# Performance work log

Measured on AMD Instinct MI355X. Metric: run time of the kernel, lower is better.

The kernel has to match this reference:

```python
import jax, jax.numpy as jnp
import numpy as np

N_EMBD = 2048
HIDDEN = 2 * N_EMBD        # 4096
ADAPT = HIDDEN // 16       # 256
B, S = 4, 2048


def _layernorm(x, g, b, eps=1e-5):
    mu = jnp.mean(x, axis=-1, keepdims=True)
    var = jnp.var(x, axis=-1, keepdims=True)
    return (x - mu) * jax.lax.rsqrt(var + eps) * g + b


def setup_inputs() -> dict:
    key = jax.random.key(0)
    ks = jax.random.split(key, 7)
    scale = 1.0 / np.sqrt(N_EMBD)
    adapt_scale = scale * 0.01
    return {
        "x": jax.random.normal(ks[0], (B, S, N_EMBD), dtype=jnp.float32),
        "W_up": jax.random.normal(ks[1], (HIDDEN, N_EMBD), dtype=jnp.float32) * scale,
        "W_gate": jax.random.normal(ks[2], (HIDDEN, N_EMBD), dtype=jnp.float32) * scale,
        "W_down": jax.random.normal(ks[3], (N_EMBD, HIDDEN), dtype=jnp.float32) * scale,
        "W_pre": jax.random.normal(ks[4], (ADAPT, N_EMBD), dtype=jnp.float32) * adapt_scale,
        "W_post": jax.random.normal(ks[5], (ADAPT, HIDDEN), dtype=jnp.float32) * adapt_scale,
        "W_proj": jax.random.normal(ks[6], (HIDDEN, ADAPT), dtype=jnp.float32) * adapt_scale,
        "ln_g": jnp.ones((ADAPT,), dtype=jnp.float32),
        "ln_b": jnp.zeros((ADAPT,), dtype=jnp.float32),
    }


def reference(x, W_up, W_gate, W_down, W_pre, W_post, W_proj, ln_g, ln_b):
    # SwiGLU trunk
    up = jnp.einsum('bsd,hd->bsh', x, W_up)
    gate = jnp.einsum('bsd,hd->bsh', x, W_gate)
    hidden = jax.nn.silu(gate) * up                      # [B,S,H]
    # Low-rank quadratic adapter
    adapt_in = _layernorm(jnp.einsum('bsd,ad->bsa', x, W_pre), ln_g, ln_b)       # [B,S,A]
    adapt_out = _layernorm(jnp.einsum('bsh,ah->bsa', hidden, W_post), ln_g, ln_b)  # [B,S,A]
    aw = jnp.einsum('bsa,bta->bst', adapt_in, adapt_out)  # [B,S,S]
    aw = jax.nn.silu(jnp.clip(aw, -5.0, 5.0))
    adapt = jnp.einsum('bst,bta->bsa', aw, adapt_in)      # [B,S,A]
    adapt = 0.1 * jnp.einsum('bsa,ha->bsh', adapt, W_proj)
    hidden = hidden + adapt
    out = jnp.einsum('bsh,dh->bsd', hidden, W_down)       # dropout p=0 -> identity
    return out
```

## Files before the change

kernel.cpp:

```cpp
#include <hip/hip_runtime.h>
#include <cstdint>
#include <cstddef>

typedef unsigned short u16;
typedef short short8 __attribute__((ext_vector_type(8)));
typedef float f32x4 __attribute__((ext_vector_type(4)));

__device__ __forceinline__ u16 f2bf(float f) {
  union { float f; unsigned u; } x; x.f = f;
  unsigned r = x.u + 0x7FFFu + ((x.u >> 16) & 1u);
  return (u16)(r >> 16);
}
__device__ __forceinline__ float b2f(u16 h) {
  union { unsigned u; float f; } x; x.u = ((unsigned)h) << 16;
  return x.f;
}
__device__ __forceinline__ float silu_f(float v) {
  return v / (1.f + __expf(-v));
}
__device__ __forceinline__ void gll(const u16* g, u16* l) {
  __builtin_amdgcn_global_load_lds((const __attribute__((address_space(1))) unsigned*)g,
                                   (__attribute__((address_space(3))) unsigned*)l, 16, 0, 0);
}
__device__ __forceinline__ short8 ld8(const u16* p) { return *(const short8*)p; }

__global__ __launch_bounds__(256) void cvt7_k(const float4* __restrict__ s0,
                                              const float4* __restrict__ s1,
                                              const float4* __restrict__ s2,
                                              const float4* __restrict__ s3,
                                              const float4* __restrict__ s4,
                                              const float4* __restrict__ s5,
                                              ushort4* __restrict__ dst) {
  const int i = blockIdx.x * 256 + threadIdx.x;
  const int o1 = 4194304, o2 = 6291456, o3 = 8388608, o4 = 10485760,
            o5 = 10616832, o6 = 10878976;
  if (i >= o6) return;
  const float4* src;
  int base;
  if      (i < o1) { src = s0; base = 0;  }
  else if (i < o2) { src = s1; base = o1; }
  else if (i < o3) { src = s2; base = o2; }
  else if (i < o4) { src = s3; base = o3; }
  else if (i < o5) { src = s4; base = o4; }
  else             { src = s5; base = o5; }
  float4 v = src[i - base];
  ushort4 o;
  o.x = f2bf(v.x); o.y = f2bf(v.y); o.z = f2bf(v.z); o.w = f2bf(v.w);
  dst[i] = o;
}

__global__ __launch_bounds__(256) void tcvt_k(const float* __restrict__ in,
                                              u16* __restrict__ out) {
  const int h = blockIdx.x, a = threadIdx.x;
  out[(size_t)a * 4096 + h] = f2bf(in[(size_t)h * 256 + a]);
}

__global__ __launch_bounds__(256) void red_ln_k(const float* __restrict__ part,
                                                const float* __restrict__ g,
                                                const float* __restrict__ b,
                                                u16* __restrict__ out,
                                                u16* __restrict__ outT, int Mtot) {
  const int row = blockIdx.x;
  const int a = threadIdx.x;
  const size_t stride = (size_t)Mtot * 256;
  const size_t base = (size_t)row * 256 + a;
  float v = part[base] + part[base + stride] + part[base + 2 * stride] + part[base + 3 * stride];
  float s = v, s2 = v * v;
#pragma unroll
  for (int o = 32; o; o >>= 1) { s += __shfl_down(s, o, 64); s2 += __shfl_down(s2, o, 64); }
  __shared__ float red[8];
  int l = a & 63, w = a >> 6;
  if (l == 0) { red[w] = s; red[4 + w] = s2; }
  __syncthreads();
  s  = red[0] + red[1] + red[2] + red[3];
  s2 = red[4] + red[5] + red[6] + red[7];
  float mu  = s * 0.00390625f;
  float var = s2 * 0.00390625f - mu * mu;
  float rs  = rsqrtf(var + 1e-5f);
  float o   = (v - mu) * rs * g[a] + b[a];
  u16 ob = f2bf(o);
  out[base] = ob;
  if (outT) {
    int bi = row >> 11, t = row & 2047;
    outT[((size_t)bi * 256 + a) * 2048 + t] = ob;
  }
}

__global__ __launch_bounds__(256) void red_k(const float* __restrict__ part,
                                             u16* __restrict__ out, int Mtot, float scale) {
  const int row = blockIdx.x;
  const int a = threadIdx.x;
  const size_t stride = (size_t)Mtot * 256;
  const size_t base = (size_t)row * 256 + a;
  float v = part[base] + part[base + stride] + part[base + 2 * stride] + part[base + 3 * stride];
  out[base] = f2bf(v * scale);
}

template <int EPI>
__global__ __launch_bounds__(256) void gemm_bt(const u16* __restrict__ A,
                                               const u16* __restrict__ B,
                                               void* __restrict__ Cv,
                                               int M, int N, int K,
                                               long bA, long bB, long bC) {
  __shared__ u16 Al[128 * 64];
  __shared__ u16 Bl[128 * 64];
  const int tid  = threadIdx.x;
  const int bz   = blockIdx.z;
  const int brow = blockIdx.y * 128;
  const int bcol = blockIdx.x * 128;
  A += (size_t)bz * bA;
  B += (size_t)bz * bB;
  const int lane = tid & 63;
  const int w = tid >> 6, wr = w >> 1, wc = w & 1;
  const int srow = tid >> 3;
  const int scol = (tid & 7) * 8;

  f32x4 acc[4][4] = {};

  for (int kt = 0; kt < K; kt += 64) {
#pragma unroll
    for (int i = 0; i < 4; ++i)
      gll(A + (size_t)(brow + i * 32 + srow) * K + kt + scol, &Al[(i * 256 + tid) * 8]);
#pragma unroll
    for (int i = 0; i < 4; ++i)
      gll(B + (size_t)(bcol + i * 32 + srow) * K + kt + scol, &Bl[(i * 256 + tid) * 8]);
    __syncthreads();
#pragma unroll
    for (int kk = 0; kk < 2; ++kk) {
      short8 af[4], bfr[4];
      const int ko = kk * 32 + (lane >> 4) * 8;
#pragma unroll
      for (int m = 0; m < 4; ++m)
        af[m] = *(const short8*)&Al[(wr * 64 + m * 16 + (lane & 15)) * 64 + ko];
#pragma unroll
      for (int n = 0; n < 4; ++n)
        bfr[n] = *(const short8*)&Bl[(wc * 64 + n * 16 + (lane & 15)) * 64 + ko];
#pragma unroll
      for (int m = 0; m < 4; ++m)
#pragma unroll
        for (int n = 0; n < 4; ++n)
          acc[m][n] = __builtin_amdgcn_mfma_f32_16x16x32_bf16(af[m], bfr[n], acc[m][n], 0, 0, 0);
    }
    __syncthreads();
  }

  const int col0 = bcol + wc * 64 + (lane & 15);
  const int row0 = brow + wr * 64 + ((lane >> 4) << 2);
  u16* Cb = (u16*)Cv + (size_t)bz * bC;
#pragma unroll
  for (int m = 0; m < 4; ++m)
#pragma unroll
    for (int j = 0; j < 4; ++j) {
      size_t roff = (size_t)(row0 + m * 16 + j) * N + col0;
#pragma unroll
      for (int n = 0; n < 4; ++n) {
        float v = acc[m][n][j];
        if (EPI == 2) {
          v = fminf(5.f, fmaxf(-5.f, v));
          v = silu_f(v);
        }
        Cb[roff + n * 16] = f2bf(v);
      }
    }
}

__global__ __launch_bounds__(256) void gemm_sk(const u16* __restrict__ A,
                                               const u16* __restrict__ B,
                                               float* __restrict__ part,
                                               int M, int N, int Kfull, int Kc,
                                               long bA, long bB, int Mtot) {
  const int z  = blockIdx.z;
  const int b  = z >> 2, sk = z & 3;
  const int brow = blockIdx.y * 128;
  const int bcol = blockIdx.x * 128;
  A += (size_t)b * bA + (size_t)sk * Kc;
  B += (size_t)b * bB + (size_t)sk * Kc;

  __shared__ u16 Al[128 * 64];
  __shared__ u16 Bl[128 * 64];
  const int tid  = threadIdx.x;
  const int lane = tid & 63;
  const int w = tid >> 6, wr = w >> 1, wc = w & 1;
  const int srow = tid >> 3;
  const int scol = (tid & 7) * 8;

  f32x4 acc[4][4] = {};

  for (int kt = 0; kt < Kc; kt += 64) {
#pragma unroll
    for (int i = 0; i < 4; ++i)
      gll(A + (size_t)(brow + i * 32 + srow) * Kfull + kt + scol, &Al[(i * 256 + tid) * 8]);
#pragma unroll
    for (int i = 0; i < 4; ++i)
      gll(B + (size_t)(bcol + i * 32 + srow) * Kfull + kt + scol, &Bl[(i * 256 + tid) * 8]);
    __syncthreads();
#pragma unroll
    for (int kk = 0; kk < 2; ++kk) {
      short8 af[4], bfr[4];
      const int ko = kk * 32 + (lane >> 4) * 8;
#pragma unroll
      for (int m = 0; m < 4; ++m)
        af[m] = *(const short8*)&Al[(wr * 64 + m * 16 + (lane & 15)) * 64 + ko];
#pragma unroll
      for (int n = 0; n < 4; ++n)
        bfr[n] = *(const short8*)&Bl[(wc * 64 + n * 16 + (lane & 15)) * 64 + ko];
#pragma unroll
      for (int m = 0; m < 4; ++m)
#pragma unroll
        for (int n = 0; n < 4; ++n)
          acc[m][n] = __builtin_amdgcn_mfma_f32_16x16x32_bf16(af[m], bfr[n], acc[m][n], 0, 0, 0);
    }
    __syncthreads();
  }

  const int col0 = bcol + wc * 64 + (lane & 15);
  const int row0 = brow + wr * 64 + ((lane >> 4) << 2);
  float* P = part + ((size_t)sk * Mtot + (size_t)b * M) * N;
#pragma unroll
  for (int m = 0; m < 4; ++m)
#pragma unroll
    for (int j = 0; j < 4; ++j) {
      size_t roff = (size_t)(row0 + m * 16 + j) * N + col0;
#pragma unroll
      for (int n = 0; n < 4; ++n) P[roff + n * 16] = acc[m][n][j];
    }
}

__device__ __forceinline__ void pipe256(const u16* Abase, const u16* Bbase, int K,
                                        u16* As, u16* Bs, int tid, int wm, int wn,
                                        int lane, f32x4 (*acc)[4]) {
  const int fr  = lane & 15;
  const int cs0 = ((((lane >> 4) << 4) ^ ((lane & 7) << 4)) >> 1);
  const int cs1 = cs0 ^ 32;
  const int NT = K >> 6;

  auto stage = [&](const u16* OPb, u16* L, int tt, int half) {
    const u16* s = OPb + (size_t)(half * 128) * K + (tt << 6);
    u16* d = &L[((tt & 1) * 2 + half) * 8192 + tid * 8];
    gll(s, d); gll(s + (size_t)64 * K, d + 4096);
  };

  stage(Abase, As, 0, 0); stage(Bbase, Bs, 0, 0);
  stage(Abase, As, 0, 1); stage(Bbase, Bs, 0, 1);
  if (NT > 1) {
    stage(Abase, As, 1, 0); stage(Bbase, Bs, 1, 0);
    stage(Abase, As, 1, 1); stage(Bbase, Bs, 1, 1);
    asm volatile("s_waitcnt vmcnt(8)" ::: "memory");
  } else {
    asm volatile("s_waitcnt vmcnt(0)" ::: "memory");
  }
  __builtin_amdgcn_s_barrier();

  const int aoff0 = (wm * 64 + fr) * 64;
  const int boff0 = (wn * 32 + fr) * 64;

  short8 aLo[8], aHi[8], bb[4];

  for (int t = 0; t < NT; ++t) {
    const u16* h0a = &As[(t & 1) * 16384];
    const u16* h0b = &Bs[(t & 1) * 16384];
    const u16* h1a = h0a + 8192;
    const u16* h1b = h0b + 8192;
    const bool pf = (t + 2 < NT);

#pragma unroll
    for (int m = 0; m < 4; ++m) {
      aLo[m * 2]     = ld8(h0a + aoff0 + m * 1024 + cs0);
      aLo[m * 2 + 1] = ld8(h0a + aoff0 + m * 1024 + cs1);
    }
#pragma unroll
    for (int n = 0; n < 2; ++n) {
      bb[n * 2]     = ld8(h0b + boff0 + n * 1024 + cs0);
      bb[n * 2 + 1] = ld8(h0b + boff0 + n * 1024 + cs1);
    }
    __builtin_amdgcn_s_barrier();
    asm volatile("s_waitcnt lgkmcnt(0)" ::: "memory");
    __builtin_amdgcn_s_setprio(1);
#pragma unroll
    for (int m = 0; m < 4; ++m)
#pragma unroll
      for (int n = 0; n < 2; ++n) {
        acc[m][n] = __builtin_amdgcn_mfma_f32_16x16x32_bf16(aLo[m*2],   bb[n*2],   acc[m][n], 0, 0, 0);
        acc[m][n] = __builtin_amdgcn_mfma_f32_16x16x32_bf16(aLo[m*2+1], bb[n*2+1], acc[m][n], 0, 0, 0);
      }
    __builtin_amdgcn_s_setprio(0);
    __builtin_amdgcn_s_barrier();

#pragma unroll
    for (int m = 0; m < 4; ++m) {
      aHi[m * 2]     = ld8(h1a + aoff0 + m * 1024 + cs0);
      aHi[m * 2 + 1] = ld8(h1a + aoff0 + m * 1024 + cs1);
    }
    if (pf) { stage(Abase, As, t + 2, 0); stage(Bbase, Bs, t + 2, 0); }
    __builtin_amdgcn_s_barrier();
    asm volatile("s_waitcnt lgkmcnt(0)" ::: "memory");
    __builtin_amdgcn_s_setprio(1);
#pragma unroll
    for (int m = 0; m < 4; ++m)
#pragma unroll
      for (int n = 0; n < 2; ++n) {
        acc[4+m][n] = __builtin_amdgcn_mfma_f32_16x16x32_bf16(aHi[m*2],   bb[n*2],   acc[4+m][n], 0, 0, 0);
        acc[4+m][n] = __builtin_amdgcn_mfma_f32_16x16x32_bf16(aHi[m*2+1], bb[n*2+1], acc[4+m][n], 0, 0, 0);
      }
    __builtin_amdgcn_s_setprio(0);
    __builtin_amdgcn_s_barrier();

#pragma unroll
    for (int n = 0; n < 2; ++n) {
      bb[n * 2]     = ld8(h1b + boff0 + n * 1024 + cs0);
      bb[n * 2 + 1] = ld8(h1b + boff0 + n * 1024 + cs1);
    }
    if (pf) stage(Abase, As, t + 2, 1);
    __builtin_amdgcn_s_barrier();
    asm volatile("s_waitcnt lgkmcnt(0)" ::: "memory");
    __builtin_amdgcn_s_setprio(1);
#pragma unroll
    for (int m = 0; m < 4; ++m)
#pragma unroll
      for (int n = 0; n < 2; ++n) {
        acc[m][2+n] = __builtin_amdgcn_mfma_f32_16x16x32_bf16(aLo[m*2],   bb[n*2],   acc[m][2+n], 0, 0, 0);
        acc[m][2+n] = __builtin_amdgcn_mfma_f32_16x16x32_bf16(aLo[m*2+1], bb[n*2+1], acc[m][2+n], 0, 0, 0);
      }
    __builtin_amdgcn_s_setprio(0);
    __builtin_amdgcn_s_barrier();

    if (pf) stage(Bbase, Bs, t + 2, 1);
    __builtin_amdgcn_s_barrier();
    asm volatile("s_waitcnt lgkmcnt(0)" ::: "memory");
    __builtin_amdgcn_s_setprio(1);
#pragma unroll
    for (int m = 0; m < 4; ++m)
#pragma unroll
      for (int n = 0; n < 2; ++n) {
        acc[4+m][2+n] = __builtin_amdgcn_mfma_f32_16x16x32_bf16(aHi[m*2],   bb[n*2],   acc[4+m][2+n], 0, 0, 0);
        acc[4+m][2+n] = __builtin_amdgcn_mfma_f32_16x16x32_bf16(aHi[m*2+1], bb[n*2+1], acc[4+m][2+n], 0, 0, 0);
      }
    __builtin_amdgcn_s_setprio(0);
    if (t + 2 < NT)      { asm volatile("s_waitcnt vmcnt(8)" ::: "memory"); }
    else if (t + 1 < NT) { asm volatile("s_waitcnt vmcnt(0)" ::: "memory"); }
    __builtin_amdgcn_s_barrier();
  }
}

template <int EPI>
__global__ __launch_bounds__(512, 2) void gemm256(const u16* __restrict__ A,
                                                  const u16* __restrict__ B,
                                                  void* __restrict__ Cv,
                                                  const u16* __restrict__ H,
                                                  int N, int K,
                                                  const u16* __restrict__ A2,
                                                  const u16* __restrict__ B2, int K2) {
  __shared__ __align__(16) u16 As[32768];
  __shared__ __align__(16) u16 Bs[32768];
  const int tid = threadIdx.x;

  const int gx = gridDim.x;
  const int nwg = gx * gridDim.y;
  int orig = blockIdx.y * gx + blockIdx.x;
  {
    int q = nwg >> 3, r = nwg & 7;
    int xcd = orig & 7, idx = orig >> 3;
    orig = (xcd < r) ? xcd * (q + 1) + idx : r * (q + 1) + (xcd - r) * q + idx;
  }
  const int brow = (orig / gx) * 256;
  const int bcol = (orig % gx) * 256;

  const int lane = tid & 63;
  const int wid  = tid >> 6;
  const int wm = wid >> 2, wn = wid & 3;
  const int srow = tid >> 3;
  const int scol = ((((tid & 7) << 4) ^ ((srow & 7) << 4)) >> 1);

  f32x4 acc[8][4] = {};

  pipe256(A + (size_t)(brow + srow) * K + scol,
          B + (size_t)(bcol + srow) * K + scol, K, As, Bs, tid, wm, wn, lane, acc);
  if (K2 > 0)
    pipe256(A2 + (size_t)(brow + srow) * K2 + scol,
            B2 + (size_t)(bcol + srow) * K2 + scol, K2, As, Bs, tid, wm, wn, lane, acc);

  const int fr = lane & 15;
#pragma unroll
  for (int m = 0; m < 8; ++m) {
    const int mrow = (m < 4) ? (wm * 64 + m * 16) : (128 + wm * 64 + (m - 4) * 16);
#pragma unroll
    for (int j = 0; j < 4; ++j) {
      const size_t roff = (size_t)(brow + mrow + ((lane >> 4) << 2) + j) * N + bcol + fr;
#pragma unroll
      for (int n = 0; n < 4; ++n) {
        const int ncol = (n < 2) ? (wn * 32 + n * 16) : (128 + wn * 32 + (n - 2) * 16);
        const size_t idx = roff + ncol;
        if (EPI == 0) {
          ((float*)Cv)[idx] = acc[m][n][j];
        } else if (EPI == 1) {
          ((u16*)Cv)[idx] = f2bf(acc[m][n][j]);
        } else {
          ((u16*)Cv)[idx] = f2bf(silu_f(acc[m][n][j]) * b2f(H[idx]));
        }
      }
    }
  }
}

extern "C" void kernel_launch(void* const* d_in, const int* in_sizes, int n_in,
                              void* d_out, int out_size, void* d_ws, size_t ws_size,
                              hipStream_t stream) {
  const float* x      = (const float*)d_in[0];
  const float* W_up   = (const float*)d_in[1];
  const float* W_gate = (const float*)d_in[2];
  const float* W_down = (const float*)d_in[3];
  const float* W_pre  = (const float*)d_in[4];
  const float* W_post = (const float*)d_in[5];
  const float* W_proj = (const float*)d_in[6];
  const float* ln_g   = (const float*)d_in[7];
  const float* ln_b   = (const float*)d_in[8];
  (void)in_sizes; (void)n_in; (void)out_size; (void)ws_size;

  const int D = 2048, Hh = 4096, A_ = 256, Bn = 4, S = 2048, M = 8192;

  char* p = (char*)d_ws;
  u16* xb      = (u16*)p; p += (size_t)M * D * 2;
  u16* Wup_b   = (u16*)p; p += (size_t)Hh * D * 2;
  u16* Wgate_b = (u16*)p; p += (size_t)Hh * D * 2;
  u16* Wdown_b = (u16*)p; p += (size_t)D * Hh * 2;
  u16* Wpre_b  = (u16*)p; p += (size_t)A_ * D * 2;
  u16* Wpost_b = (u16*)p; p += (size_t)A_ * Hh * 2;
  u16* WprojT  = (u16*)p; p += (size_t)Hh * A_ * 2;
  u16* hidden  = (u16*)p; p += (size_t)M * Hh * 2;
  u16* scratch = (u16*)p; p += (size_t)M * Hh * 2;
  char* q = (char*)scratch;
  u16*   aw        = (u16*)q; q += (size_t)Bn * S * S * 2;
  u16*   adapt_in  = (u16*)q; q += (size_t)M * A_ * 2;
  u16*   adapt_inT = (u16*)q; q += (size_t)M * A_ * 2;
  u16*   adapt_out = (u16*)q; q += (size_t)M * A_ * 2;
  u16*   adaptb    = (u16*)q; q += (size_t)M * A_ * 2;
  float* wdp_part  = (float*)q; q += (size_t)4 * 2048 * 256 * 4;
  u16*   Wdp_b     = (u16*)q; q += (size_t)2048 * 256 * 2;
  float* part = (float*)Wup_b;

  cvt7_k<<<dim3(42496), dim3(256), 0, stream>>>((const float4*)x, (const float4*)W_up,
                                                (const float4*)W_gate, (const float4*)W_down,
                                                (const float4*)W_pre, (const float4*)W_post,
                                                (ushort4*)xb);
  tcvt_k<<<dim3(4096), dim3(256), 0, stream>>>(W_proj, WprojT);

  gemm_sk<<<dim3(A_ / 128, 2048 / 128, 4), 256, 0, stream>>>(Wdown_b, WprojT, wdp_part,
                                                             2048, A_, Hh, Hh / 4, 0, 0, 2048);
  red_k<<<dim3(2048), 256, 0, stream>>>(wdp_part, Wdp_b, 2048, 0.1f);

  gemm256<1><<<dim3(Hh / 256, M / 256), 512, 0, stream>>>(xb, Wup_b, hidden, nullptr,
                                                          Hh, D, nullptr, nullptr, 0);
  gemm256<4><<<dim3(Hh / 256, M / 256), 512, 0, stream>>>(xb, Wgate_b, hidden, hidden,
                                                          Hh, D, nullptr, nullptr, 0);

  gemm_sk<<<dim3(A_ / 128, M / 128, 4), 256, 0, stream>>>(xb, Wpre_b, part,
                                                          M, A_, D, D / 4, 0, 0, M);
  red_ln_k<<<dim3(M), 256, 0, stream>>>(part, ln_g, ln_b, adapt_in, adapt_inT, M);

  gemm_sk<<<dim3(A_ / 128, M / 128, 4), 256, 0, stream>>>(hidden, Wpost_b, part,
                                                          M, A_, Hh, Hh / 4, 0, 0, M);
  red_ln_k<<<dim3(M), 256, 0, stream>>>(part, ln_g, ln_b, adapt_out, nullptr, M);

  gemm_bt<2><<<dim3(S / 128, S / 128, Bn), 256, 0, stream>>>(adapt_in, adapt_out, aw,
                                                             S, S, A_,
                                                             (long)S * A_, (long)S * A_, (long)S * S);

  gemm_sk<<<dim3(A_ / 128, S / 128, Bn * 4), 256, 0, stream>>>(aw, adapt_inT, part,
                                                               S, A_, S, S / 4,
                                                               (long)S * S, (long)A_ * S, M);
  red_k<<<dim3(M), 256, 0, stream>>>(part, adaptb, M, 1.0f);

  gemm256<0><<<dim3(D / 256, M / 256), 512, 0, stream>>>(hidden, Wdown_b, d_out, nullptr,
                                                         D, Hh, adaptb, Wdp_b, A_);
}
```

Measured before the change: 605.6 us.

## Fuse up and gate GEMMs into one kernel, swizzle LDS in small GEMMs

The separate up and gate GEMMs, where the gate pass re-read hidden to apply silu(gate)*up, are merged into one gemm256 variant. Each block loads 128 up rows and 128 matching gate rows, with W_up and W_gate stored back to back and addressed through a half offset, and writes the SwiGLU product once. This removes a full bf16 round trip of hidden and one launch. The gemm_sk and gemm_bt kernels gain an XOR swizzle on LDS columns to cut bank conflicts. The W_down·W_proj split-K is widened to 8 splits, with its partials buffer moved into the hidden region.

```diff
diff --git a/kernel.cpp b/kernel.cpp
--- a/kernel.cpp
+++ b/kernel.cpp
@@ -86,13 +86,16 @@
   }
 }
 
+template <int SK>
 __global__ __launch_bounds__(256) void red_k(const float* __restrict__ part,
                                              u16* __restrict__ out, int Mtot, float scale) {
   const int row = blockIdx.x;
   const int a = threadIdx.x;
   const size_t stride = (size_t)Mtot * 256;
   const size_t base = (size_t)row * 256 + a;
-  float v = part[base] + part[base + stride] + part[base + 2 * stride] + part[base + 3 * stride];
+  float v = 0.f;
+#pragma unroll
+  for (int s = 0; s < SK; ++s) v += part[base + (size_t)s * stride];
   out[base] = f2bf(v * scale);
 }
 
@@ -113,7 +116,9 @@
   const int lane = tid & 63;
   const int w = tid >> 6, wr = w >> 1, wc = w & 1;
   const int srow = tid >> 3;
-  const int scol = (tid & 7) * 8;
+  const int scol = (((tid & 7) ^ (srow & 7)) * 8);
+  const int fr   = lane & 15;
+  const int kg   = lane >> 4;
 
   f32x4 acc[4][4] = {};
 
@@ -128,13 +133,17 @@
 #pragma unroll
     for (int kk = 0; kk < 2; ++kk) {
       short8 af[4], bfr[4];
-      const int ko = kk * 32 + (lane >> 4) * 8;
-#pragma unroll
-      for (int m = 0; m < 4; ++m)
-        af[m] = *(const short8*)&Al[(wr * 64 + m * 16 + (lane & 15)) * 64 + ko];
-#pragma unroll
-      for (int n = 0; n < 4; ++n)
-        bfr[n] = *(const short8*)&Bl[(wc * 64 + n * 16 + (lane & 15)) * 64 + ko];
+      const int ko8 = kk * 4 + kg;
+#pragma unroll
+      for (int m = 0; m < 4; ++m) {
+        const int r = wr * 64 + m * 16 + fr;
+        af[m] = ld8(&Al[r * 64 + ((ko8 ^ (fr & 7)) << 3)]);
+      }
+#pragma unroll
+      for (int n = 0; n < 4; ++n) {
+        const int r = wc * 64 + n * 16 + fr;
+        bfr[n] = ld8(&Bl[r * 64 + ((ko8 ^ (fr & 7)) << 3)]);
+      }
 #pragma unroll
       for (int m = 0; m < 4; ++m)
 #pragma unroll
@@ -144,8 +153,8 @@
     __syncthreads();
   }
 
-  const int col0 = bcol + wc * 64 + (lane & 15);
-  const int row0 = brow + wr * 64 + ((lane >> 4) << 2);
+  const int col0 = bcol + wc * 64 + fr;
+  const int row0 = brow + wr * 64 + (kg << 2);
   u16* Cb = (u16*)Cv + (size_t)bz * bC;
 #pragma unroll
   for (int m = 0; m < 4; ++m)
@@ -164,13 +173,14 @@
     }
 }
 
+template <int SK>
 __global__ __launch_bounds__(256) void gemm_sk(const u16* __restrict__ A,
                                                const u16* __restrict__ B,
                                                float* __restrict__ part,
                                                int M, int N, int Kfull, int Kc,
                                                long bA, long bB, int Mtot) {
   const int z  = blockIdx.z;
-  const int b  = z >> 2, sk = z & 3;
+  const int b  = z / SK, sk = z % SK;
   const int brow = blockIdx.y * 128;
   const int bcol = blockIdx.x * 128;
   A += (size_t)b * bA + (size_t)sk * Kc;
@@ -182,7 +192,9 @@
   const int lane = tid & 63;
   const int w = tid >> 6, wr = w >> 1, wc = w & 1;
   const int srow = tid >> 3;
-  const int scol = (tid & 7) * 8;
+  const int scol = (((tid & 7) ^ (srow & 7)) * 8);
+  const int fr   = lane & 15;
+  const int kg   = lane >> 4;
 
   f32x4 acc[4][4] = {};
 
@@ -197,13 +209,17 @@
 #pragma unroll
     for (int kk = 0; kk < 2; ++kk) {
       short8 af[4], bfr[4];
-      const int ko = kk * 32 + (lane >> 4) * 8;
-#pragma unroll
-      for (int m = 0; m < 4; ++m)
-        af[m] = *(const short8*)&Al[(wr * 64 + m * 16 + (lane & 15)) * 64 + ko];
-#pragma unroll
-      for (int n = 0; n < 4; ++n)
-        bfr[n] = *(const short8*)&Bl[(wc * 64 + n * 16 + (lane & 15)) * 64 + ko];
+      const int ko8 = kk * 4 + kg;
+#pragma unroll
+      for (int m = 0; m < 4; ++m) {
+        const int r = wr * 64 + m * 16 + fr;
+        af[m] = ld8(&Al[r * 64 + ((ko8 ^ (fr & 7)) << 3)]);
+      }
+#pragma unroll
+      for (int n = 0; n < 4; ++n) {
+        const int r = wc * 64 + n * 16 + fr;
+        bfr[n] = ld8(&Bl[r * 64 + ((ko8 ^ (fr & 7)) << 3)]);
+      }
 #pragma unroll
       for (int m = 0; m < 4; ++m)
 #pragma unroll
@@ -213,8 +229,8 @@
     __syncthreads();
   }
 
-  const int col0 = bcol + wc * 64 + (lane & 15);
-  const int row0 = brow + wr * 64 + ((lane >> 4) << 2);
+  const int col0 = bcol + wc * 64 + fr;
+  const int row0 = brow + wr * 64 + (kg << 2);
   float* P = part + ((size_t)sk * Mtot + (size_t)b * M) * N;
 #pragma unroll
   for (int m = 0; m < 4; ++m)
@@ -228,23 +244,28 @@
 
 __device__ __forceinline__ void pipe256(const u16* Abase, const u16* Bbase, int K,
                                         u16* As, u16* Bs, int tid, int wm, int wn,
-                                        int lane, f32x4 (*acc)[4]) {
+                                        int lane, f32x4 (*acc)[4], int bHalfOff) {
   const int fr  = lane & 15;
   const int cs0 = ((((lane >> 4) << 4) ^ ((lane & 7) << 4)) >> 1);
   const int cs1 = cs0 ^ 32;
   const int NT = K >> 6;
 
-  auto stage = [&](const u16* OPb, u16* L, int tt, int half) {
-    const u16* s = OPb + (size_t)(half * 128) * K + (tt << 6);
-    u16* d = &L[((tt & 1) * 2 + half) * 8192 + tid * 8];
+  auto stageA = [&](int tt, int half) {
+    const u16* s = Abase + (size_t)(half * 128) * K + (tt << 6);
+    u16* d = &As[((tt & 1) * 2 + half) * 8192 + tid * 8];
     gll(s, d); gll(s + (size_t)64 * K, d + 4096);
   };
-
-  stage(Abase, As, 0, 0); stage(Bbase, Bs, 0, 0);
-  stage(Abase, As, 0, 1); stage(Bbase, Bs, 0, 1);
+  auto stageB = [&](int tt, int half) {
+    const u16* s = Bbase + (size_t)half * bHalfOff * K + (tt << 6);
+    u16* d = &Bs[((tt & 1) * 2 + half) * 8192 + tid * 8];
+    gll(s, d); gll(s + (size_t)64 * K, d + 4096);
+  };
+
+  stageA(0, 0); stageB(0, 0);
+  stageA(0, 1); stageB(0, 1);
   if (NT > 1) {
-    stage(Abase, As, 1, 0); stage(Bbase, Bs, 1, 0);
-    stage(Abase, As, 1, 1); stage(Bbase, Bs, 1, 1);
+    stageA(1, 0); stageB(1, 0);
+    stageA(1, 1); stageB(1, 1);
     asm volatile("s_waitcnt vmcnt(8)" ::: "memory");
   } else {
     asm volatile("s_waitcnt vmcnt(0)" ::: "memory");
@@ -291,7 +312,7 @@
       aHi[m * 2]     = ld8(h1a + aoff0 + m * 1024 + cs0);
       aHi[m * 2 + 1] = ld8(h1a + aoff0 + m * 1024 + cs1);
     }
-    if (pf) { stage(Abase, As, t + 2, 0); stage(Bbase, Bs, t + 2, 0); }
+    if (pf) { stageA(t + 2, 0); stageB(t + 2, 0); }
     __builtin_amdgcn_s_barrier();
     asm volatile("s_waitcnt lgkmcnt(0)" ::: "memory");
     __builtin_amdgcn_s_setprio(1);
@@ -310,7 +331,7 @@
       bb[n * 2]     = ld8(h1b + boff0 + n * 1024 + cs0);
       bb[n * 2 + 1] = ld8(h1b + boff0 + n * 1024 + cs1);
     }
-    if (pf) stage(Abase, As, t + 2, 1);
+    if (pf) stageA(t + 2, 1);
     __builtin_amdgcn_s_barrier();
     asm volatile("s_waitcnt lgkmcnt(0)" ::: "memory");
     __builtin_amdgcn_s_setprio(1);
@@ -324,7 +345,7 @@
     __builtin_amdgcn_s_setprio(0);
     __builtin_amdgcn_s_barrier();
 
-    if (pf) stage(Bbase, Bs, t + 2, 1);
+    if (pf) stageB(t + 2, 1);
     __builtin_amdgcn_s_barrier();
     asm volatile("s_waitcnt lgkmcnt(0)" ::: "memory");
     __builtin_amdgcn_s_setprio(1);
@@ -346,7 +367,6 @@
 __global__ __launch_bounds__(512, 2) void gemm256(const u16* __restrict__ A,
                                                   const u16* __restrict__ B,
                                                   void* __restrict__ Cv,
-                                                  const u16* __restrict__ H,
                                                   int N, int K,
                                                   const u16* __restrict__ A2,
                                                   const u16* __restrict__ B2, int K2) {
@@ -363,7 +383,8 @@
     orig = (xcd < r) ? xcd * (q + 1) + idx : r * (q + 1) + (xcd - r) * q + idx;
   }
   const int brow = (orig / gx) * 256;
-  const int bcol = (orig % gx) * 256;
+  const int bcol = (orig % gx) * ((EPI == 5) ? 128 : 256);
+  const int bHalfOff = (EPI == 5) ? 4096 : 128;
 
   const int lane = tid & 63;
   const int wid  = tid >> 6;
@@ -374,29 +395,37 @@
   f32x4 acc[8][4] = {};
 
   pipe256(A + (size_t)(brow + srow) * K + scol,
-          B + (size_t)(bcol + srow) * K + scol, K, As, Bs, tid, wm, wn, lane, acc);
+          B + (size_t)(bcol + srow) * K + scol, K, As, Bs, tid, wm, wn, lane, acc, bHalfOff);
   if (K2 > 0)
     pipe256(A2 + (size_t)(brow + srow) * K2 + scol,
-            B2 + (size_t)(bcol + srow) * K2 + scol, K2, As, Bs, tid, wm, wn, lane, acc);
+            B2 + (size_t)(bcol + srow) * K2 + scol, K2, As, Bs, tid, wm, wn, lane, acc, 128);
 
   const int fr = lane & 15;
-#pragma unroll
-  for (int m = 0; m < 8; ++m) {
-    const int mrow = (m < 4) ? (wm * 64 + m * 16) : (128 + wm * 64 + (m - 4) * 16);
-#pragma unroll
-    for (int j = 0; j < 4; ++j) {
-      const size_t roff = (size_t)(brow + mrow + ((lane >> 4) << 2) + j) * N + bcol + fr;
-#pragma unroll
-      for (int n = 0; n < 4; ++n) {
-        const int ncol = (n < 2) ? (wn * 32 + n * 16) : (128 + wn * 32 + (n - 2) * 16);
-        const size_t idx = roff + ncol;
-        if (EPI == 0) {
-          ((float*)Cv)[idx] = acc[m][n][j];
-        } else if (EPI == 1) {
-          ((u16*)Cv)[idx] = f2bf(acc[m][n][j]);
-        } else {
-          ((u16*)Cv)[idx] = f2bf(silu_f(acc[m][n][j]) * b2f(H[idx]));
+  if (EPI == 0) {
+#pragma unroll
+    for (int m = 0; m < 8; ++m) {
+      const int mrow = (m < 4) ? (wm * 64 + m * 16) : (128 + wm * 64 + (m - 4) * 16);
+#pragma unroll
+      for (int j = 0; j < 4; ++j) {
+        const size_t roff = (size_t)(brow + mrow + ((lane >> 4) << 2) + j) * N + bcol + fr;
+#pragma unroll
+        for (int n = 0; n < 4; ++n) {
+          const int ncol = (n < 2) ? (wn * 32 + n * 16) : (128 + wn * 32 + (n - 2) * 16);
+          ((float*)Cv)[roff + ncol] = acc[m][n][j];
         }
+      }
+    }
+  } else {
+    u16* Cb = (u16*)Cv;
+#pragma unroll
+    for (int m = 0; m < 8; ++m) {
+      const int mrow = (m < 4) ? (wm * 64 + m * 16) : (128 + wm * 64 + (m - 4) * 16);
+#pragma unroll
+      for (int j = 0; j < 4; ++j) {
+        const size_t roff = (size_t)(brow + mrow + ((lane >> 4) << 2) + j) * N + bcol + wn * 32 + fr;
+#pragma unroll
+        for (int n = 0; n < 2; ++n)
+          Cb[roff + n * 16] = f2bf(silu_f(acc[m][n + 2][j]) * acc[m][n][j]);
       }
     }
   }
@@ -420,8 +449,7 @@
 
   char* p = (char*)d_ws;
   u16* xb      = (u16*)p; p += (size_t)M * D * 2;
-  u16* Wup_b   = (u16*)p; p += (size_t)Hh * D * 2;
-  u16* Wgate_b = (u16*)p; p += (size_t)Hh * D * 2;
+  u16* Wug_b   = (u16*)p; p += (size_t)2 * Hh * D * 2;
   u16* Wdown_b = (u16*)p; p += (size_t)D * Hh * 2;
   u16* Wpre_b  = (u16*)p; p += (size_t)A_ * D * 2;
   u16* Wpost_b = (u16*)p; p += (size_t)A_ * Hh * 2;
@@ -434,9 +462,9 @@
   u16*   adapt_inT = (u16*)q; q += (size_t)M * A_ * 2;
   u16*   adapt_out = (u16*)q; q += (size_t)M * A_ * 2;
   u16*   adaptb    = (u16*)q; q += (size_t)M * A_ * 2;
-  float* wdp_part  = (float*)q; q += (size_t)4 * 2048 * 256 * 4;
   u16*   Wdp_b     = (u16*)q; q += (size_t)2048 * 256 * 2;
-  float* part = (float*)Wup_b;
+  float* part     = (float*)Wug_b;
+  float* wdp_part = (float*)hidden;
 
   cvt7_k<<<dim3(42496), dim3(256), 0, stream>>>((const float4*)x, (const float4*)W_up,
                                                 (const float4*)W_gate, (const float4*)W_down,
@@ -444,32 +472,30 @@
                                                 (ushort4*)xb);
   tcvt_k<<<dim3(4096), dim3(256), 0, stream>>>(W_proj, WprojT);
 
-  gemm_sk<<<dim3(A_ / 128, 2048 / 128, 4), 256, 0, stream>>>(Wdown_b, WprojT, wdp_part,
-                                                             2048, A_, Hh, Hh / 4, 0, 0, 2048);
-  red_k<<<dim3(2048), 256, 0, stream>>>(wdp_part, Wdp_b, 2048, 0.1f);
-
-  gemm256<1><<<dim3(Hh / 256, M / 256), 512, 0, stream>>>(xb, Wup_b, hidden, nullptr,
+  gemm_sk<8><<<dim3(A_ / 128, 2048 / 128, 8), 256, 0, stream>>>(Wdown_b, WprojT, wdp_part,
+                                                                2048, A_, Hh, Hh / 8, 0, 0, 2048);
+  red_k<8><<<dim3(2048), 256, 0, stream>>>(wdp_part, Wdp_b, 2048, 0.1f);
+
+  gemm256<5><<<dim3(Hh / 128, M / 256), 512, 0, stream>>>(xb, Wug_b, hidden,
                                                           Hh, D, nullptr, nullptr, 0);
-  gemm256<4><<<dim3(Hh / 256, M / 256), 512, 0, stream>>>(xb, Wgate_b, hidden, hidden,
-                                                          Hh, D, nullptr, nullptr, 0);
-
-  gemm_sk<<<dim3(A_ / 128, M / 128, 4), 256, 0, stream>>>(xb, Wpre_b, part,
-                                                          M, A_, D, D / 4, 0, 0, M);
+
+  gemm_sk<4><<<dim3(A_ / 128, M / 128, 4), 256, 0, stream>>>(xb, Wpre_b, part,
+                                                             M, A_, D, D / 4, 0, 0, M);
   red_ln_k<<<dim3(M), 256, 0, stream>>>(part, ln_g, ln_b, adapt_in, adapt_inT, M);
 
-  gemm_sk<<<dim3(A_ / 128, M / 128, 4), 256, 0, stream>>>(hidden, Wpost_b, part,
-                                                          M, A_, Hh, Hh / 4, 0, 0, M);
+  gemm_sk<4><<<dim3(A_ / 128, M / 128, 4), 256, 0, stream>>>(hidden, Wpost_b, part,
+                                                             M, A_, Hh, Hh / 4, 0, 0, M);
   red_ln_k<<<dim3(M), 256, 0, stream>>>(part, ln_g, ln_b, adapt_out, nullptr, M);
 
   gemm_bt<2><<<dim3(S / 128, S / 128, Bn), 256, 0, stream>>>(adapt_in, adapt_out, aw,
                                                              S, S, A_,
                                                              (long)S * A_, (long)S * A_, (long)S * S);
 
-  gemm_sk<<<dim3(A_ / 128, S / 128, Bn * 4), 256, 0, stream>>>(aw, adapt_inT, part,
-                                                               S, A_, S, S / 4,
-                                                               (long)S * S, (long)A_ * S, M);
-  red_k<<<dim3(M), 256, 0, stream>>>(part, adaptb, M, 1.0f);
-
-  gemm256<0><<<dim3(D / 256, M / 256), 512, 0, stream>>>(hidden, Wdown_b, d_out, nullptr,
+  gemm_sk<4><<<dim3(A_ / 128, S / 128, Bn * 4), 256, 0, stream>>>(aw, adapt_inT, part,
+                                                                  S, A_, S, S / 4,
+                                                                  (long)S * S, (long)A_ * S, M);
+  red_k<4><<<dim3(M), 256, 0, stream>>>(part, adaptb, M, 1.0f);
+
+  gemm256<0><<<dim3(D / 256, M / 256), 512, 0, stream>>>(hidden, Wdown_b, d_out,
                                                          D, Hh, adaptb, Wdp_b, A_);
 }
```

After: 593.3 us. 2.0% less time.
